# Optimization experiments

Measured on AMD Instinct MI355X. Metric: run time of the kernel, lower is better.

The kernel has to match this reference:

```python
import jax, jax.numpy as jnp
import numpy as np

N_NODES, N_EDGES = 512, 4096
P_OBJ, P_REL = 512, 256
D_NODE = D_EDGE = 256
H_GNN = 512
N_LAYERS = 2
N_OBJ_CLS, N_REL_CLS = 160, 26


def _pointnet(x, w1, b1, w2, b2, w3, b3):
    # x: [B, C_in, P] point cloud; pointwise conv1d == per-point MLP, then max-pool over points
    h = jax.nn.relu(jnp.einsum('bcp,cd->bpd', x, w1) + b1)
    h = jax.nn.relu(jnp.einsum('bpc,cd->bpd', h, w2) + b2)
    h = jnp.einsum('bpc,cd->bpd', h, w3) + b3
    return h.max(axis=1)  # [B, D]


def _mlp3(x, w1, b1, w2, b2, w3, b3):
    h = jax.nn.relu(x @ w1 + b1)
    h = jax.nn.relu(h @ w2 + b2)
    return h @ w3 + b3


def setup_inputs() -> dict:
    key = jax.random.key(0)
    ks = iter(jax.random.split(key, 64))

    def w(shape):
        fan = shape[-2]
        return jax.random.normal(next(ks), shape, dtype=jnp.float32) / np.float32(np.sqrt(fan))

    def b(shape):
        return jnp.zeros(shape, jnp.float32)

    d3 = 2 * D_NODE + D_EDGE  # triplet concat dim
    inp = dict(
        obj_points=jax.random.normal(next(ks), (N_NODES, 3, P_OBJ), dtype=jnp.float32),
        rel_points=jax.random.normal(next(ks), (N_EDGES, 4, P_REL), dtype=jnp.float32),
        edge_index=jax.random.randint(next(ks), (2, N_EDGES), 0, N_NODES),
        obj_w1=w((3, 64)), obj_b1=b((64,)), obj_w2=w((64, 128)), obj_b2=b((128,)),
        obj_w3=w((128, D_NODE)), obj_b3=b((D_NODE,)),
        rel_w1=w((4, 64)), rel_b1=b((64,)), rel_w2=w((64, 128)), rel_b2=b((128,)),
        rel_w3=w((128, D_EDGE)), rel_b3=b((D_EDGE,)),
        g_tw1=w((N_LAYERS, d3, H_GNN)), g_tb1=b((N_LAYERS, H_GNN)),
        g_tw2=w((N_LAYERS, H_GNN, d3)), g_tb2=b((N_LAYERS, d3)),
        g_nw1=w((N_LAYERS, D_NODE, H_GNN)), g_nb1=b((N_LAYERS, H_GNN)),
        g_nw2=w((N_LAYERS, H_GNN, D_NODE)), g_nb2=b((N_LAYERS, D_NODE)),
        oc_w1=w((D_NODE, 512)), oc_b1=b((512,)), oc_w2=w((512, 256)), oc_b2=b((256,)),
        oc_w3=w((256, N_OBJ_CLS)), oc_b3=b((N_OBJ_CLS,)),
        rc_w1=w((D_EDGE, 512)), rc_b1=b((512,)), rc_w2=w((512, 256)), rc_b2=b((256,)),
        rc_w3=w((256, N_REL_CLS)), rc_b3=b((N_REL_CLS,)),
    )
    return inp


def reference(obj_points, rel_points, edge_index,
              obj_w1, obj_b1, obj_w2, obj_b2, obj_w3, obj_b3,
              rel_w1, rel_b1, rel_w2, rel_b2, rel_w3, rel_b3,
              g_tw1, g_tb1, g_tw2, g_tb2, g_nw1, g_nb1, g_nw2, g_nb2,
              oc_w1, oc_b1, oc_w2, oc_b2, oc_w3, oc_b3,
              rc_w1, rc_b1, rc_w2, rc_b2, rc_w3, rc_b3):
    # PointNet encoders
    x = _pointnet(obj_points, obj_w1, obj_b1, obj_w2, obj_b2, obj_w3, obj_b3)  # [N, Dn]
    e = _pointnet(rel_points, rel_w1, rel_b1, rel_w2, rel_b2, rel_w3, rel_b3)  # [E, De]
    s, o = edge_index[0], edge_index[1]
    ones = jnp.ones((N_EDGES, 1), x.dtype)
    # Triplet GNN (GraphTripleConv-style message passing)
    for l in range(N_LAYERS):
        t = jnp.concatenate([x[s], e, x[o]], axis=-1)                 # [E, 2Dn+De]
        h = jax.nn.relu(t @ g_tw1[l] + g_tb1[l]) @ g_tw2[l] + g_tb2[l]
        ns = h[:, :D_NODE]
        ne = h[:, D_NODE:D_NODE + D_EDGE]
        no = h[:, D_NODE + D_EDGE:]
        pooled = (jax.ops.segment_sum(ns, s, num_segments=N_NODES)
                  + jax.ops.segment_sum(no, o, num_segments=N_NODES))
        cnt = (jax.ops.segment_sum(ones, s, num_segments=N_NODES)
               + jax.ops.segment_sum(ones, o, num_segments=N_NODES))
        avg = pooled / jnp.maximum(cnt, 1.0)                          # scatter-mean
        x = jax.nn.relu(avg @ g_nw1[l] + g_nb1[l]) @ g_nw2[l] + g_nb2[l]
        e = ne
    obj_cls = jax.nn.log_softmax(
        _mlp3(x, oc_w1, oc_b1, oc_w2, oc_b2, oc_w3, oc_b3), axis=-1)  # PointNetCls
    rel_cls = jax.nn.sigmoid(
        _mlp3(e, rc_w1, rc_b1, rc_w2, rc_b2, rc_w3, rc_b3))           # PointNetRelClsMulti
    return (obj_cls, rel_cls)
```

## Files before the change

### kernel.cpp

```cpp
#include <hip/hip_runtime.h>
#include <hip/hip_bf16.h>
#include <math.h>

#define N_NODES 512
#define N_EDGES 4096
#define D_NODE 256
#define D3 768
#define H_GNN 512
#define N_OBJ_CLS 160
#define N_REL_CLS 26

typedef __attribute__((ext_vector_type(8))) short bf16x8;
typedef __attribute__((ext_vector_type(4))) float f32x4;

__device__ __forceinline__ unsigned short f2bf(float x) {
  unsigned u = __float_as_uint(x);
  u = u + 0x7FFFu + ((u >> 16) & 1u);
  return (unsigned short)(u >> 16);
}
__device__ __forceinline__ float bf2f(unsigned short h) {
  return __uint_as_float(((unsigned)h) << 16);
}
__device__ __forceinline__ unsigned cvtpk(float a, float b) {
  __hip_bfloat162 h = __float22bfloat162_rn(make_float2(a, b));
  return *reinterpret_cast<unsigned*>(&h);
}

struct WEnt { const float* src; unsigned short* dh; unsigned short* dl; int K; int N; int start; };
struct WBatch { WEnt e[18]; int total; };

__global__ __launch_bounds__(256) void wtrans_batch(WBatch wb) {
  int idx = blockIdx.x * 256 + threadIdx.x;
  const int stride = gridDim.x * 256;
  for (; idx < wb.total; idx += stride) {
    int i = 0;
#pragma unroll
    for (int t = 1; t < 18; ++t) if (idx >= wb.e[t].start) i = t;
    const int local = idx - wb.e[i].start;
    const int K = wb.e[i].K;
    const int n = local / K, k = local - n * K;
    const float v = wb.e[i].src[k * wb.e[i].N + n];
    const unsigned short hi = f2bf(v);
    wb.e[i].dh[local] = hi;
    wb.e[i].dl[local] = f2bf(v - bf2f(hi));
  }
}

template<int CIN, int PTOT, int NSPLIT>
__global__ __launch_bounds__(256) void pointnet_mfma(
    const float* __restrict__ in,
    const float* __restrict__ w1, const float* __restrict__ b1,
    const unsigned short* __restrict__ w2t, const float* __restrict__ b2,
    const unsigned short* __restrict__ w3t, const float* __restrict__ b3,
    unsigned short* __restrict__ outh,
    float* __restrict__ pmax)
{
  constexpr int PBLK = PTOT / NSPLIT;
  __shared__ unsigned short h1h[64][72];
  __shared__ unsigned short h2h[64][136];
  const int tid = threadIdx.x;
  const int wv = tid >> 6, l = tid & 63, lr = l & 15, lg = l >> 4;
  const int blk = blockIdx.x;
  const int b  = blk / NSPLIT;
  const int sp = blk % NSPLIT;
  const float* inb = in + (size_t)b * CIN * PTOT + (size_t)sp * PBLK;

  const int chA = 2 * (l & 31);
  const int sub = l >> 5;
  float w1c0[CIN], w1c1[CIN];
#pragma unroll
  for (int c = 0; c < CIN; ++c) {
    w1c0[c] = w1[c * 64 + chA];
    w1c1[c] = w1[c * 64 + chA + 1];
  }
  const float b1v0 = b1[chA], b1v1 = b1[chA + 1];

  bf16x8 w2f[2][2];
#pragma unroll
  for (int mt = 0; mt < 2; ++mt)
#pragma unroll
    for (int kt = 0; kt < 2; ++kt)
      w2f[mt][kt] = *(const bf16x8*)(w2t + (size_t)(32 * wv + mt * 16 + lr) * 64 + kt * 32 + lg * 8);
  bf16x8 w3f[4][4];
#pragma unroll
  for (int mt = 0; mt < 4; ++mt)
#pragma unroll
    for (int kt = 0; kt < 4; ++kt)
      w3f[mt][kt] = *(const bf16x8*)(w3t + (size_t)(64 * wv + mt * 16 + lr) * 128 + kt * 32 + lg * 8);

  float4 b2v[2];
#pragma unroll
  for (int mt = 0; mt < 2; ++mt)
    b2v[mt] = *(const float4*)&b2[32 * wv + mt * 16 + lg * 4];

  f32x4 mxf[4];
#pragma unroll
  for (int mt = 0; mt < 4; ++mt) { f32x4 z = {-INFINITY, -INFINITY, -INFINITY, -INFINITY}; mxf[mt] = z; }

  for (int t0 = 0; t0 < PBLK; t0 += 64) {
    {
      const int pl0 = wv * 16 + sub * 8;
      float4 xv0[CIN], xv1[CIN];
#pragma unroll
      for (int c = 0; c < CIN; ++c) {
        xv0[c] = *(const float4*)&inb[c * PTOT + t0 + pl0];
        xv1[c] = *(const float4*)&inb[c * PTOT + t0 + pl0 + 4];
      }
#pragma unroll
      for (int pp = 0; pp < 8; ++pp) {
        float a0 = b1v0, a1 = b1v1;
#pragma unroll
        for (int c = 0; c < CIN; ++c) {
          const float xc = (pp < 4) ? ((const float*)&xv0[c])[pp]
                                    : ((const float*)&xv1[c])[pp - 4];
          a0 = fmaf(xc, w1c0[c], a0);
          a1 = fmaf(xc, w1c1[c], a1);
        }
        a0 = fmaxf(a0, 0.f); a1 = fmaxf(a1, 0.f);
        *(unsigned*)&h1h[pl0 + pp][chA] = cvtpk(a0, a1);
      }
    }
    __syncthreads();
#pragma unroll
    for (int ntt = 0; ntt < 4; ++ntt) {
      bf16x8 bh[2];
#pragma unroll
      for (int kt = 0; kt < 2; ++kt)
        bh[kt] = *(const bf16x8*)&h1h[ntt * 16 + lr][kt * 32 + lg * 8];
#pragma unroll
      for (int mt = 0; mt < 2; ++mt) {
        f32x4 a = {0.f, 0.f, 0.f, 0.f};
#pragma unroll
        for (int kt = 0; kt < 2; ++kt)
          a = __builtin_amdgcn_mfma_f32_16x16x32_bf16(w2f[mt][kt], bh[kt], a, 0, 0, 0);
        const float v0 = fmaxf(a[0] + b2v[mt].x, 0.f);
        const float v1 = fmaxf(a[1] + b2v[mt].y, 0.f);
        const float v2 = fmaxf(a[2] + b2v[mt].z, 0.f);
        const float v3 = fmaxf(a[3] + b2v[mt].w, 0.f);
        const int pr = ntt * 16 + lr, cc = 32 * wv + mt * 16 + lg * 4;
        *(uint2*)&h2h[pr][cc] = make_uint2(cvtpk(v0, v1), cvtpk(v2, v3));
      }
    }
    __syncthreads();
#pragma unroll
    for (int ntt = 0; ntt < 4; ++ntt) {
      bf16x8 ah[4];
#pragma unroll
      for (int kt = 0; kt < 4; ++kt)
        ah[kt] = *(const bf16x8*)&h2h[ntt * 16 + lr][kt * 32 + lg * 8];
#pragma unroll
      for (int mt = 0; mt < 4; ++mt) {
        f32x4 a = {0.f, 0.f, 0.f, 0.f};
#pragma unroll
        for (int kt = 0; kt < 4; ++kt)
          a = __builtin_amdgcn_mfma_f32_16x16x32_bf16(w3f[mt][kt], ah[kt], a, 0, 0, 0);
#pragma unroll
        for (int j = 0; j < 4; ++j) mxf[mt][j] = fmaxf(mxf[mt][j], a[j]);
      }
    }
    __syncthreads();
  }
#pragma unroll
  for (int mt = 0; mt < 4; ++mt)
#pragma unroll
    for (int j = 0; j < 4; ++j) {
      float v = mxf[mt][j];
      v = fmaxf(v, __shfl_xor(v, 1));
      v = fmaxf(v, __shfl_xor(v, 2));
      v = fmaxf(v, __shfl_xor(v, 4));
      v = fmaxf(v, __shfl_xor(v, 8));
      mxf[mt][j] = v;
    }
  if (lr == 0) {
    if (NSPLIT == 1) {
#pragma unroll
      for (int mt = 0; mt < 4; ++mt) {
        const int ch = 64 * wv + mt * 16 + lg * 4;
        const float4 b3v = *(const float4*)&b3[ch];
        const size_t o = (size_t)b * 256 + ch;
        *(uint2*)(outh + o) = make_uint2(cvtpk(mxf[mt][0] + b3v.x, mxf[mt][1] + b3v.y),
                                         cvtpk(mxf[mt][2] + b3v.z, mxf[mt][3] + b3v.w));
      }
    } else {
#pragma unroll
      for (int mt = 0; mt < 4; ++mt) {
        const int ch = 64 * wv + mt * 16 + lg * 4;
        const size_t o = ((size_t)b * NSPLIT + sp) * 256 + ch;
        *(float4*)&pmax[o] = make_float4(mxf[mt][0], mxf[mt][1], mxf[mt][2], mxf[mt][3]);
      }
    }
  }
}

template<int NSPLIT>
__global__ __launch_bounds__(256) void combine_max(
    const float* __restrict__ pmax, const float* __restrict__ b3,
    unsigned short* __restrict__ outh)
{
  const int b = blockIdx.x, ch = threadIdx.x;
  float m = pmax[(size_t)b * NSPLIT * 256 + ch];
#pragma unroll
  for (int s = 1; s < NSPLIT; ++s)
    m = fmaxf(m, pmax[((size_t)b * NSPLIT + s) * 256 + ch]);
  outh[(size_t)b * 256 + ch] = f2bf(m + b3[ch]);
}

template<int ACT, int OUT, bool GATHER>
__global__ __launch_bounds__(256) void mgemm(
    const unsigned short* __restrict__ Ah, int lda,
    const unsigned short* __restrict__ Eh,
    const int* __restrict__ ei,
    const unsigned short* __restrict__ Wh, const unsigned short* __restrict__ Wl,
    const float* __restrict__ bias,
    unsigned short* __restrict__ Oh, int ldo,
    float* __restrict__ Of, float* __restrict__ pooled,
    int M, int N, int K)
{
  __shared__ unsigned short sAh[64][72];
  __shared__ unsigned short sBh[64][72], sBl[64][72];
  __shared__ int sS[64], sO[64];
  const int tid = threadIdx.x;
  const int wv = tid >> 6, l = tid & 63, lr = l & 15, lg = l >> 4;
  const int wm = wv >> 1, wn = wv & 1;
  const int bm = blockIdx.y * 64, bn = blockIdx.x * 64;
  const int srow = tid >> 3;
  const int sch  = (tid & 7) * 8;

  if ((GATHER || OUT == 2) && tid < 64) {
    sS[tid] = ei[bm + tid];
    sO[tid] = ei[N_EDGES + bm + tid];
  }
  __syncthreads();

  float bv[2];
#pragma unroll
  for (int ni = 0; ni < 2; ++ni) {
    const int col = bn + wn * 32 + ni * 16 + lr;
    bv[ni] = (col < N) ? bias[col] : 0.f;
  }

  f32x4 acc[2][2];
#pragma unroll
  for (int mi = 0; mi < 2; ++mi)
#pragma unroll
    for (int ni = 0; ni < 2; ++ni) { f32x4 z = {0.f, 0.f, 0.f, 0.f}; acc[mi][ni] = z; }

  const int nsteps = K >> 6;

  auto loadA = [&](int k0, int it) -> bf16x8 {
    const int r = it * 32 + srow;
    const unsigned short* ph;
    if (GATHER) {
      const int kg = k0 + sch;
      if (kg < 256)      ph = Ah + (size_t)sS[r] * 256 + kg;
      else if (kg < 512) ph = Eh + (size_t)(bm + r) * 256 + (kg - 256);
      else               ph = Ah + (size_t)sO[r] * 256 + (kg - 512);
    } else {
      ph = Ah + (size_t)(bm + r) * lda + k0 + sch;
    }
    return *(const bf16x8*)ph;
  };
  auto loadB = [&](const unsigned short* W, int k0, int it) -> bf16x8 {
    int n = bn + it * 32 + srow;
    if (n >= N) n = N - 1;
    return *(const bf16x8*)(W + (size_t)n * K + k0 + sch);
  };

  bf16x8 rA[2], rBh[2], rBl[2];
#pragma unroll
  for (int it = 0; it < 2; ++it) {
    rA[it]  = loadA(0, it);
    rBh[it] = loadB(Wh, 0, it);
    rBl[it] = loadB(Wl, 0, it);
  }

  for (int t = 0; t < nsteps; ++t) {
    __syncthreads();
#pragma unroll
    for (int it = 0; it < 2; ++it) {
      *(bf16x8*)&sAh[it * 32 + srow][sch] = rA[it];
      *(bf16x8*)&sBh[it * 32 + srow][sch] = rBh[it];
      *(bf16x8*)&sBl[it * 32 + srow][sch] = rBl[it];
    }
    __syncthreads();
    if (t + 1 < nsteps) {
      const int k1 = (t + 1) << 6;
#pragma unroll
      for (int it = 0; it < 2; ++it) {
        rA[it]  = loadA(k1, it);
        rBh[it] = loadB(Wh, k1, it);
        rBl[it] = loadB(Wl, k1, it);
      }
    }
#pragma unroll
    for (int kt = 0; kt < 2; ++kt) {
      bf16x8 afh[2], bfh[2], bfl[2];
#pragma unroll
      for (int mi = 0; mi < 2; ++mi)
        afh[mi] = *(const bf16x8*)&sAh[wm * 32 + mi * 16 + lr][kt * 32 + lg * 8];
#pragma unroll
      for (int ni = 0; ni < 2; ++ni) {
        bfh[ni] = *(const bf16x8*)&sBh[wn * 32 + ni * 16 + lr][kt * 32 + lg * 8];
        bfl[ni] = *(const bf16x8*)&sBl[wn * 32 + ni * 16 + lr][kt * 32 + lg * 8];
      }
#pragma unroll
      for (int mi = 0; mi < 2; ++mi)
#pragma unroll
        for (int ni = 0; ni < 2; ++ni) {
          acc[mi][ni] = __builtin_amdgcn_mfma_f32_16x16x32_bf16(afh[mi], bfh[ni], acc[mi][ni], 0, 0, 0);
          acc[mi][ni] = __builtin_amdgcn_mfma_f32_16x16x32_bf16(afh[mi], bfl[ni], acc[mi][ni], 0, 0, 0);
        }
    }
  }
#pragma unroll
  for (int mi = 0; mi < 2; ++mi)
#pragma unroll
    for (int ni = 0; ni < 2; ++ni) {
      const int colb = bn + wn * 32 + ni * 16 + lr;
#pragma unroll
      for (int j = 0; j < 4; ++j) {
        const int lrow = wm * 32 + mi * 16 + lg * 4 + j;
        float v = acc[mi][ni][j] + bv[ni];
        if (ACT == 1) v = fmaxf(v, 0.f);
        else if (ACT == 2) v = 1.f / (1.f + expf(-v));
        if (OUT == 0) {
          if (colb < N) Oh[(size_t)(bm + lrow) * ldo + colb] = f2bf(v);
        } else if (OUT == 1) {
          if (colb < N) Of[(size_t)(bm + lrow) * ldo + colb] = v;
        } else {
          if (colb < 256) {
            atomicAdd(&pooled[(size_t)sS[lrow] * 256 + colb], v);
          } else if (colb < 512) {
            Oh[(size_t)(bm + lrow) * 256 + (colb - 256)] = f2bf(v);
          } else {
            atomicAdd(&pooled[(size_t)sO[lrow] * 256 + (colb - 512)], v);
          }
        }
      }
    }
}

__global__ __launch_bounds__(256) void count_kernel(const int* __restrict__ ei,
                                                    float* __restrict__ cnt)
{
  const int i = blockIdx.x * blockDim.x + threadIdx.x;
  if (i < 2 * N_EDGES) atomicAdd(&cnt[ei[i]], 1.0f);
}

__global__ __launch_bounds__(256) void avg_plane_kernel(const float* __restrict__ pooled,
                                                        const float* __restrict__ cnt,
                                                        unsigned short* __restrict__ ah)
{
  const int i = blockIdx.x * 256 + threadIdx.x;
  ah[i] = f2bf(pooled[i] / fmaxf(cnt[i >> 8], 1.0f));
}

__global__ __launch_bounds__(256) void logsoftmax_kernel(const float* __restrict__ logits,
                                                         float* __restrict__ out)
{
  __shared__ float red[256];
  const int r = blockIdx.x, tid = threadIdx.x;
  const float v = (tid < N_OBJ_CLS) ? logits[(size_t)r * N_OBJ_CLS + tid] : -INFINITY;
  red[tid] = v;
  __syncthreads();
  for (int s = 128; s > 0; s >>= 1) {
    if (tid < s) red[tid] = fmaxf(red[tid], red[tid + s]);
    __syncthreads();
  }
  const float mxv = red[0];
  __syncthreads();
  red[tid] = (tid < N_OBJ_CLS) ? expf(v - mxv) : 0.0f;
  __syncthreads();
  for (int s = 128; s > 0; s >>= 1) {
    if (tid < s) red[tid] += red[tid + s];
    __syncthreads();
  }
  const float lse = mxv + logf(red[0]);
  if (tid < N_OBJ_CLS) out[(size_t)r * N_OBJ_CLS + tid] = v - lse;
}

extern "C" void kernel_launch(void* const* d_in, const int* in_sizes, int n_in,
                              void* d_out, int out_size, void* d_ws, size_t ws_size,
                              hipStream_t stream)
{
  const float* obj_points = (const float*)d_in[0];
  const float* rel_points = (const float*)d_in[1];
  const int*   edge_index = (const int*)d_in[2];
  const float* obj_w1 = (const float*)d_in[3];
  const float* obj_b1 = (const float*)d_in[4];
  const float* obj_w2 = (const float*)d_in[5];
  const float* obj_b2 = (const float*)d_in[6];
  const float* obj_w3 = (const float*)d_in[7];
  const float* obj_b3 = (const float*)d_in[8];
  const float* rel_w1 = (const float*)d_in[9];
  const float* rel_b1 = (const float*)d_in[10];
  const float* rel_w2 = (const float*)d_in[11];
  const float* rel_b2 = (const float*)d_in[12];
  const float* rel_w3 = (const float*)d_in[13];
  const float* rel_b3 = (const float*)d_in[14];
  const float* g_tw1 = (const float*)d_in[15];
  const float* g_tb1 = (const float*)d_in[16];
  const float* g_tw2 = (const float*)d_in[17];
  const float* g_tb2 = (const float*)d_in[18];
  const float* g_nw1 = (const float*)d_in[19];
  const float* g_nb1 = (const float*)d_in[20];
  const float* g_nw2 = (const float*)d_in[21];
  const float* g_nb2 = (const float*)d_in[22];
  const float* oc_w1 = (const float*)d_in[23];
  const float* oc_b1 = (const float*)d_in[24];
  const float* oc_w2 = (const float*)d_in[25];
  const float* oc_b2 = (const float*)d_in[26];
  const float* oc_w3 = (const float*)d_in[27];
  const float* oc_b3 = (const float*)d_in[28];
  const float* rc_w1 = (const float*)d_in[29];
  const float* rc_b1 = (const float*)d_in[30];
  const float* rc_w2 = (const float*)d_in[31];
  const float* rc_b2 = (const float*)d_in[32];
  const float* rc_w3 = (const float*)d_in[33];
  const float* rc_b3 = (const float*)d_in[34];
  float* out = (float*)d_out;

  unsigned short* u = (unsigned short*)d_ws;
  size_t uo = 0;
  auto UA = [&](size_t n) { unsigned short* p = u + uo; uo += n; return p; };
  unsigned short* x0h = UA(131072);
  unsigned short* x1h = UA(131072);
  unsigned short* e0h = UA(1048576);
  unsigned short* neh = UA(1048576);
  unsigned short* h1h = UA(2097152);
  unsigned short* avgh = UA(131072);
  unsigned short* nhh = UA(262144);
  unsigned short* ow2h = UA(8192);   unsigned short* ow2l = UA(8192);
  unsigned short* ow3h = UA(32768);  unsigned short* ow3l = UA(32768);
  unsigned short* rw2h = UA(8192);   unsigned short* rw2l = UA(8192);
  unsigned short* rw3h = UA(32768);  unsigned short* rw3l = UA(32768);
  unsigned short* tw1h[2], *tw1l[2], *tw2h[2], *tw2l[2], *nw1h[2], *nw1l[2], *nw2h[2], *nw2l[2];
  for (int i = 0; i < 2; ++i) { tw1h[i] = UA(393216); tw1l[i] = UA(393216); }
  for (int i = 0; i < 2; ++i) { tw2h[i] = UA(393216); tw2l[i] = UA(393216); }
  for (int i = 0; i < 2; ++i) { nw1h[i] = UA(131072); nw1l[i] = UA(131072); }
  for (int i = 0; i < 2; ++i) { nw2h[i] = UA(131072); nw2l[i] = UA(131072); }
  unsigned short* oc1h = UA(131072); unsigned short* oc1l = UA(131072);
  unsigned short* oc2h = UA(131072); unsigned short* oc2l = UA(131072);
  unsigned short* oc3h = UA(40960);  unsigned short* oc3l = UA(40960);
  unsigned short* rc1h = UA(131072); unsigned short* rc1l = UA(131072);
  unsigned short* rc2h = UA(131072); unsigned short* rc2l = UA(131072);
  unsigned short* rc3h = UA(6656);   unsigned short* rc3l = UA(6656);
  float* f = (float*)(u + ((uo + 7) & ~(size_t)7));
  float* pooled = f;
  float* cntf   = f + 131072;
  float* logits = f + 131584;
  float* pmax   = f + 213504;
  unsigned short* hh1h = h1h;
  unsigned short* hh2h = e0h;

  WBatch wb;
  int cum = 0, wi = 0;
  auto ADD = [&](const float* src, unsigned short* dh, unsigned short* dl, int K, int N) {
    wb.e[wi].src = src; wb.e[wi].dh = dh; wb.e[wi].dl = dl;
    wb.e[wi].K = K; wb.e[wi].N = N; wb.e[wi].start = cum;
    cum += K * N; ++wi;
  };
  ADD(obj_w2, ow2h, ow2l, 64, 128);
  ADD(obj_w3, ow3h, ow3l, 128, 256);
  ADD(rel_w2, rw2h, rw2l, 64, 128);
  ADD(rel_w3, rw3h, rw3l, 128, 256);
  for (int i = 0; i < 2; ++i) ADD(g_tw1 + (size_t)i * 393216, tw1h[i], tw1l[i], 768, 512);
  for (int i = 0; i < 2; ++i) ADD(g_tw2 + (size_t)i * 393216, tw2h[i], tw2l[i], 512, 768);
  for (int i = 0; i < 2; ++i) ADD(g_nw1 + (size_t)i * 131072, nw1h[i], nw1l[i], 256, 512);
  for (int i = 0; i < 2; ++i) ADD(g_nw2 + (size_t)i * 131072, nw2h[i], nw2l[i], 512, 256);
  ADD(oc_w1, oc1h, oc1l, 256, 512);
  ADD(oc_w2, oc2h, oc2l, 512, 256);
  ADD(oc_w3, oc3h, oc3l, 256, 160);
  ADD(rc_w1, rc1h, rc1l, 256, 512);
  ADD(rc_w2, rc2h, rc2l, 512, 256);
  ADD(rc_w3, rc3h, rc3l, 256, 26);
  wb.total = cum;
  wtrans_batch<<<4096, 256, 0, stream>>>(wb);

  pointnet_mfma<3, 512, 4><<<N_NODES * 4, 256, 0, stream>>>(
      obj_points, obj_w1, obj_b1, ow2h, obj_b2, ow3h, obj_b3, nullptr, pmax);
  combine_max<4><<<N_NODES, 256, 0, stream>>>(pmax, obj_b3, x0h);
  pointnet_mfma<4, 256, 1><<<N_EDGES, 256, 0, stream>>>(
      rel_points, rel_w1, rel_b1, rw2h, rel_b2, rw3h, rel_b3, e0h, nullptr);

  hipMemsetAsync(cntf, 0, 512 * sizeof(float), stream);
  count_kernel<<<32, 256, 0, stream>>>(edge_index, cntf);

  unsigned short *xch = x0h, *xnh = x1h;
  unsigned short *ech = e0h;
  for (int ll = 0; ll < 2; ++ll) {
    mgemm<1, 0, true><<<dim3(8, 64), 256, 0, stream>>>(
        xch, 256, ech, edge_index, tw1h[ll], tw1l[ll], g_tb1 + ll * H_GNN,
        h1h, 512, nullptr, nullptr, N_EDGES, H_GNN, D3);
    hipMemsetAsync(pooled, 0, (size_t)N_NODES * D_NODE * sizeof(float), stream);
    mgemm<0, 2, false><<<dim3(12, 64), 256, 0, stream>>>(
        h1h, 512, nullptr, edge_index, tw2h[ll], tw2l[ll], g_tb2 + ll * D3,
        neh, 256, nullptr, pooled, N_EDGES, D3, H_GNN);
    avg_plane_kernel<<<512, 256, 0, stream>>>(pooled, cntf, avgh);
    mgemm<1, 0, false><<<dim3(8, 8), 256, 0, stream>>>(
        avgh, 256, nullptr, nullptr, nw1h[ll], nw1l[ll], g_nb1 + ll * H_GNN,
        nhh, 512, nullptr, nullptr, N_NODES, H_GNN, D_NODE);
    mgemm<0, 0, false><<<dim3(4, 8), 256, 0, stream>>>(
        nhh, 512, nullptr, nullptr, nw2h[ll], nw2l[ll], g_nb2 + ll * D_NODE,
        xnh, 256, nullptr, nullptr, N_NODES, D_NODE, H_GNN);
    unsigned short* t = xch; xch = xnh; xnh = t;
    ech = neh;
  }

  mgemm<1, 0, false><<<dim3(8, 8), 256, 0, stream>>>(
      xch, 256, nullptr, nullptr, oc1h, oc1l, oc_b1,
      hh1h, 512, nullptr, nullptr, N_NODES, 512, 256);
  mgemm<1, 0, false><<<dim3(4, 8), 256, 0, stream>>>(
      hh1h, 512, nullptr, nullptr, oc2h, oc2l, oc_b2,
      hh2h, 256, nullptr, nullptr, N_NODES, 256, 512);
  mgemm<0, 1, false><<<dim3(3, 8), 256, 0, stream>>>(
      hh2h, 256, nullptr, nullptr, oc3h, oc3l, oc_b3,
      nullptr, N_OBJ_CLS, logits, nullptr, N_NODES, N_OBJ_CLS, 256);
  logsoftmax_kernel<<<N_NODES, 256, 0, stream>>>(logits, out);

  mgemm<1, 0, false><<<dim3(8, 64), 256, 0, stream>>>(
      ech, 256, nullptr, nullptr, rc1h, rc1l, rc_b1,
      hh1h, 512, nullptr, nullptr, N_EDGES, 512, 256);
  mgemm<1, 0, false><<<dim3(4, 64), 256, 0, stream>>>(
      hh1h, 512, nullptr, nullptr, rc2h, rc2l, rc_b2,
      hh2h, 256, nullptr, nullptr, N_EDGES, 256, 512);
  mgemm<2, 1, false><<<dim3(1, 64), 256, 0, stream>>>(
      hh2h, 256, nullptr, nullptr, rc3h, rc3l, rc_b3,
      nullptr, N_REL_CLS, out + (size_t)N_NODES * N_OBJ_CLS, nullptr,
      N_EDGES, N_REL_CLS, 256);
}
```

Measured before the change: 294.0 us.

## Horizontally fuse pointnets, edge counting, and classifier head GEMMs into shared launches

Merges the object and relation PointNet kernels and the edge-count scatter into one launch with interleaved block roles, raising object point split from 4 to 8. Pairs the object and relation classifier MLP layers into combined launches so the small node GEMMs run alongside the edge GEMMs. This removes several kernel launches and fills the GPU better during the small head GEMMs, at the cost of heterogeneous blocks sharing one kernel's resource footprint and more partial-max traffic.

```diff
diff --git a/kernel.cpp b/kernel.cpp
--- a/kernel.cpp
+++ b/kernel.cpp
@@ -47,20 +47,20 @@
 }
 
 template<int CIN, int PTOT, int NSPLIT>
-__global__ __launch_bounds__(256) void pointnet_mfma(
+__device__ __forceinline__ void pn_body(
+    int blk,
     const float* __restrict__ in,
     const float* __restrict__ w1, const float* __restrict__ b1,
     const unsigned short* __restrict__ w2t, const float* __restrict__ b2,
     const unsigned short* __restrict__ w3t, const float* __restrict__ b3,
     unsigned short* __restrict__ outh,
-    float* __restrict__ pmax)
+    float* __restrict__ pmax,
+    unsigned short (&h1h)[64][72],
+    unsigned short (&h2h)[64][136])
 {
   constexpr int PBLK = PTOT / NSPLIT;
-  __shared__ unsigned short h1h[64][72];
-  __shared__ unsigned short h2h[64][136];
   const int tid = threadIdx.x;
   const int wv = tid >> 6, l = tid & 63, lr = l & 15, lg = l >> 4;
-  const int blk = blockIdx.x;
   const int b  = blk / NSPLIT;
   const int sp = blk % NSPLIT;
   const float* inb = in + (size_t)b * CIN * PTOT + (size_t)sp * PBLK;
@@ -192,6 +192,35 @@
   }
 }
 
+__global__ __launch_bounds__(256) void pointnets_fused(
+    const float* __restrict__ obj_in,
+    const float* __restrict__ ow1, const float* __restrict__ ob1,
+    const unsigned short* __restrict__ ow2t, const float* __restrict__ ob2,
+    const unsigned short* __restrict__ ow3t, const float* __restrict__ ob3,
+    float* __restrict__ pmax,
+    const float* __restrict__ rel_in,
+    const float* __restrict__ rw1, const float* __restrict__ rb1,
+    const unsigned short* __restrict__ rw2t, const float* __restrict__ rb2,
+    const unsigned short* __restrict__ rw3t, const float* __restrict__ rb3,
+    unsigned short* __restrict__ e_outh,
+    const int* __restrict__ ei, float* __restrict__ cnt)
+{
+  __shared__ unsigned short h1h[64][72];
+  __shared__ unsigned short h2h[64][136];
+  const int bid = blockIdx.x;
+  if (bid < 8192) {
+    if (bid & 1)
+      pn_body<4, 256, 1>(bid >> 1, rel_in, rw1, rb1, rw2t, rb2, rw3t, rb3,
+                         e_outh, nullptr, h1h, h2h);
+    else
+      pn_body<3, 512, 8>(bid >> 1, obj_in, ow1, ob1, ow2t, ob2, ow3t, ob3,
+                         nullptr, pmax, h1h, h2h);
+  } else {
+    const int i = (bid - 8192) * 256 + threadIdx.x;
+    if (i < 2 * N_EDGES) atomicAdd(&cnt[ei[i]], 1.0f);
+  }
+}
+
 template<int NSPLIT>
 __global__ __launch_bounds__(256) void combine_max(
     const float* __restrict__ pmax, const float* __restrict__ b3,
@@ -206,7 +235,7 @@
 }
 
 template<int ACT, int OUT, bool GATHER>
-__global__ __launch_bounds__(256) void mgemm(
+__device__ __forceinline__ void mgemm_body(
     const unsigned short* __restrict__ Ah, int lda,
     const unsigned short* __restrict__ Eh,
     const int* __restrict__ ei,
@@ -214,7 +243,7 @@
     const float* __restrict__ bias,
     unsigned short* __restrict__ Oh, int ldo,
     float* __restrict__ Of, float* __restrict__ pooled,
-    int M, int N, int K)
+    int M, int N, int K, int bx, int by)
 {
   __shared__ unsigned short sAh[64][72];
   __shared__ unsigned short sBh[64][72], sBl[64][72];
@@ -222,7 +251,7 @@
   const int tid = threadIdx.x;
   const int wv = tid >> 6, l = tid & 63, lr = l & 15, lg = l >> 4;
   const int wm = wv >> 1, wn = wv & 1;
-  const int bm = blockIdx.y * 64, bn = blockIdx.x * 64;
+  const int bm = by * 64, bn = bx * 64;
   const int srow = tid >> 3;
   const int sch  = (tid & 7) * 8;
 
@@ -340,11 +369,60 @@
     }
 }
 
-__global__ __launch_bounds__(256) void count_kernel(const int* __restrict__ ei,
-                                                    float* __restrict__ cnt)
-{
-  const int i = blockIdx.x * blockDim.x + threadIdx.x;
-  if (i < 2 * N_EDGES) atomicAdd(&cnt[ei[i]], 1.0f);
+template<int ACT, int OUT, bool GATHER>
+__global__ __launch_bounds__(256) void mgemm(
+    const unsigned short* __restrict__ Ah, int lda,
+    const unsigned short* __restrict__ Eh,
+    const int* __restrict__ ei,
+    const unsigned short* __restrict__ Wh, const unsigned short* __restrict__ Wl,
+    const float* __restrict__ bias,
+    unsigned short* __restrict__ Oh, int ldo,
+    float* __restrict__ Of, float* __restrict__ pooled,
+    int M, int N, int K)
+{
+  mgemm_body<ACT, OUT, GATHER>(Ah, lda, Eh, ei, Wh, Wl, bias, Oh, ldo, Of, pooled,
+                               M, N, K, blockIdx.x, blockIdx.y);
+}
+
+__global__ __launch_bounds__(256) void head12_fused(
+    const unsigned short* __restrict__ rA, int rlda,
+    const unsigned short* __restrict__ rWh, const unsigned short* __restrict__ rWl,
+    const float* __restrict__ rbias, unsigned short* __restrict__ rO, int rldo,
+    int rM, int rN, int rK, int rGX, int rGY,
+    const unsigned short* __restrict__ oA, int olda,
+    const unsigned short* __restrict__ oWh, const unsigned short* __restrict__ oWl,
+    const float* __restrict__ obias, unsigned short* __restrict__ oO, int oldo,
+    int oM, int oN, int oK, int oGX)
+{
+  int b = blockIdx.x;
+  const int nrel = rGX * rGY;
+  if (b < nrel)
+    mgemm_body<1, 0, false>(rA, rlda, nullptr, nullptr, rWh, rWl, rbias,
+                            rO, rldo, nullptr, nullptr, rM, rN, rK, b % rGX, b / rGX);
+  else {
+    b -= nrel;
+    mgemm_body<1, 0, false>(oA, olda, nullptr, nullptr, oWh, oWl, obias,
+                            oO, oldo, nullptr, nullptr, oM, oN, oK, b % oGX, b / oGX);
+  }
+}
+
+__global__ __launch_bounds__(256) void head3_fused(
+    const unsigned short* __restrict__ rA,
+    const unsigned short* __restrict__ rWh, const unsigned short* __restrict__ rWl,
+    const float* __restrict__ rbias, float* __restrict__ rOf,
+    const unsigned short* __restrict__ oA,
+    const unsigned short* __restrict__ oWh, const unsigned short* __restrict__ oWl,
+    const float* __restrict__ obias, float* __restrict__ oOf)
+{
+  int b = blockIdx.x;
+  if (b < 64)
+    mgemm_body<2, 1, false>(rA, 256, nullptr, nullptr, rWh, rWl, rbias,
+                            nullptr, N_REL_CLS, rOf, nullptr, N_EDGES, N_REL_CLS, 256, 0, b);
+  else {
+    b -= 64;
+    mgemm_body<0, 1, false>(oA, 256, nullptr, nullptr, oWh, oWl, obias,
+                            nullptr, N_OBJ_CLS, oOf, nullptr, N_NODES, N_OBJ_CLS, 256, b % 3, b / 3);
+  }
 }
 
 __global__ __launch_bounds__(256) void avg_plane_kernel(const float* __restrict__ pooled,
@@ -430,6 +508,8 @@
   unsigned short* h1h = UA(2097152);
   unsigned short* avgh = UA(131072);
   unsigned short* nhh = UA(262144);
+  unsigned short* oh1 = UA(262144);
+  unsigned short* oh2 = UA(131072);
   unsigned short* ow2h = UA(8192);   unsigned short* ow2l = UA(8192);
   unsigned short* ow3h = UA(32768);  unsigned short* ow3l = UA(32768);
   unsigned short* rw2h = UA(8192);   unsigned short* rw2l = UA(8192);
@@ -475,16 +555,14 @@
   ADD(rc_w2, rc2h, rc2l, 512, 256);
   ADD(rc_w3, rc3h, rc3l, 256, 26);
   wb.total = cum;
+  hipMemsetAsync(cntf, 0, 512 * sizeof(float), stream);
   wtrans_batch<<<4096, 256, 0, stream>>>(wb);
 
-  pointnet_mfma<3, 512, 4><<<N_NODES * 4, 256, 0, stream>>>(
-      obj_points, obj_w1, obj_b1, ow2h, obj_b2, ow3h, obj_b3, nullptr, pmax);
-  combine_max<4><<<N_NODES, 256, 0, stream>>>(pmax, obj_b3, x0h);
-  pointnet_mfma<4, 256, 1><<<N_EDGES, 256, 0, stream>>>(
-      rel_points, rel_w1, rel_b1, rw2h, rel_b2, rw3h, rel_b3, e0h, nullptr);
-
-  hipMemsetAsync(cntf, 0, 512 * sizeof(float), stream);
-  count_kernel<<<32, 256, 0, stream>>>(edge_index, cntf);
+  pointnets_fused<<<8224, 256, 0, stream>>>(
+      obj_points, obj_w1, obj_b1, ow2h, obj_b2, ow3h, obj_b3, pmax,
+      rel_points, rel_w1, rel_b1, rw2h, rel_b2, rw3h, rel_b3, e0h,
+      edge_index, cntf);
+  combine_max<8><<<N_NODES, 256, 0, stream>>>(pmax, obj_b3, x0h);
 
   unsigned short *xch = x0h, *xnh = x1h;
   unsigned short *ech = e0h;
@@ -507,25 +585,14 @@
     ech = neh;
   }
 
-  mgemm<1, 0, false><<<dim3(8, 8), 256, 0, stream>>>(
-      xch, 256, nullptr, nullptr, oc1h, oc1l, oc_b1,
-      hh1h, 512, nullptr, nullptr, N_NODES, 512, 256);
-  mgemm<1, 0, false><<<dim3(4, 8), 256, 0, stream>>>(
-      hh1h, 512, nullptr, nullptr, oc2h, oc2l, oc_b2,
-      hh2h, 256, nullptr, nullptr, N_NODES, 256, 512);
-  mgemm<0, 1, false><<<dim3(3, 8), 256, 0, stream>>>(
-      hh2h, 256, nullptr, nullptr, oc3h, oc3l, oc_b3,
-      nullptr, N_OBJ_CLS, logits, nullptr, N_NODES, N_OBJ_CLS, 256);
+  head12_fused<<<512 + 64, 256, 0, stream>>>(
+      ech, 256, rc1h, rc1l, rc_b1, hh1h, 512, N_EDGES, 512, 256, 8, 64,
+      xch, 256, oc1h, oc1l, oc_b1, oh1, 512, N_NODES, 512, 256, 8);
+  head12_fused<<<256 + 32, 256, 0, stream>>>(
+      hh1h, 512, rc2h, rc2l, rc_b2, hh2h, 256, N_EDGES, 256, 512, 4, 64,
+      oh1, 512, oc2h, oc2l, oc_b2, oh2, 256, N_NODES, 256, 512, 4);
+  head3_fused<<<64 + 24, 256, 0, stream>>>(
+      hh2h, rc3h, rc3l, rc_b3, out + (size_t)N_NODES * N_OBJ_CLS,
+      oh2, oc3h, oc3l, oc_b3, logits);
   logsoftmax_kernel<<<N_NODES, 256, 0, stream>>>(logits, out);
-
-  mgemm<1, 0, false><<<dim3(8, 64), 256, 0, stream>>>(
-      ech, 256, nullptr, nullptr, rc1h, rc1l, rc_b1,
-      hh1h, 512, nullptr, nullptr, N_EDGES, 512, 256);
-  mgemm<1, 0, false><<<dim3(4, 64), 256, 0, stream>>>(
-      hh1h, 512, nullptr, nullptr, rc2h, rc2l, rc_b2,
-      hh2h, 256, nullptr, nullptr, N_EDGES, 256, 512);
-  mgemm<2, 1, false><<<dim3(1, 64), 256, 0, stream>>>(
-      hh2h, 256, nullptr, nullptr, rc3h, rc3l, rc_b3,
-      nullptr, N_REL_CLS, out + (size_t)N_NODES * N_OBJ_CLS, nullptr,
-      N_EDGES, N_REL_CLS, 256);
-}
+}
```

After: 396.6 us. 1.35x slower.
